# Kernel tuning notes

Hardware: AMD Instinct MI355X
Metric: run time of the kernel (lower is better)

The kernel has to match this reference:

```python
import jax, jax.numpy as jnp
import numpy as np

DIM = 1024
N_QUBITS = 10
NUM_LAYERS = 4
BATCH = 32768


def _build_cyclic_cnot(n_qubits):
    # Faithful replication of the torch build (which swaps each row pair
    # twice per control, so the result is the identity matrix).
    dim = 2 ** n_qubits
    cnot = np.eye(dim, dtype=np.float32)
    for control in range(n_qubits - 1):
        target = control + 1
        for i in range(dim):
            if (i >> control) & 1:
                j = i ^ (1 << target)
                cnot[[i, j], :] = cnot[[j, i], :]
    control, target = n_qubits - 1, 0
    for i in range(dim):
        if (i >> control) & 1:
            j = i ^ (1 << target)
            cnot[[i, j], :] = cnot[[j, i], :]
    return cnot


def setup_inputs() -> dict:
    key = jax.random.key(0)
    kx, ka = jax.random.split(key)
    x = jax.random.normal(kx, (BATCH, DIM), dtype=jnp.float32)
    local_angles = jax.random.normal(ka, (NUM_LAYERS, N_QUBITS, 3), dtype=jnp.float32)
    cnot_matrix = jnp.asarray(_build_cyclic_cnot(N_QUBITS))
    return {"x": x, "local_angles": local_angles, "cnot_matrix": cnot_matrix}


def _single_qubit_gates(angles):
    # angles: (L, n, 3) -> per-qubit 2x2 gate Rz @ Ry @ Rx, each R(t)=[[c,-s],[s,c]]
    h = angles * 0.5
    c, s = jnp.cos(h), jnp.sin(h)
    R = jnp.stack([jnp.stack([c, -s], axis=-1),
                   jnp.stack([s, c], axis=-1)], axis=-2)  # (L, n, 3, 2, 2)
    return jnp.einsum('lnij,lnjk,lnkm->lnim', R[:, :, 2], R[:, :, 1], R[:, :, 0])  # (L, n, 2, 2)


def _kron_all(mats):
    # mats: (n, 2, 2) -> dense (2^n, 2^n) Kronecker product, qubit 0 outermost
    out = mats[0]
    for q in range(1, mats.shape[0]):
        d = out.shape[0]
        out = jnp.einsum('ij,kl->ikjl', out, mats[q]).reshape(d * 2, d * 2)
    return out


def reference(x, local_angles, cnot_matrix):
    gates = _single_qubit_gates(local_angles)  # (L, n, 2, 2)
    out = x
    for l in range(local_angles.shape[0]):
        U = _kron_all(gates[l])  # (dim, dim)
        out = out @ U.T
        out = out @ cnot_matrix.T
    return out
```

## Files before the change

kernel.cpp:

```cpp
#include <hip/hip_runtime.h>
#include <math.h>

#define WPB 4
#define LDS_STRIDE 1184

__device__ __forceinline__ int padA(int i) {
    return i + ((i >> 5) << 2) + (((i >> 8) & 3) << 3) + (((i >> 6) & 3) << 2);
}

#define LGKM0() __asm__ volatile("s_waitcnt lgkmcnt(0)" ::: "memory")

__global__ __launch_bounds__(256) void qel_butterfly(
    const float* __restrict__ x,
    const float* __restrict__ ang,
    float* __restrict__ out,
    int rows)
{
    __shared__ __align__(16) float sm[WPB * LDS_STRIDE];
    const int tid  = threadIdx.x;
    const int wave = tid >> 6;
    const int lane = tid & 63;
    float* wsm = sm + wave * LDS_STRIDE;

    float cb[10], sb[10];
#pragma unroll
    for (int n = 0; n < 10; ++n) {
        float t = 0.f;
#pragma unroll
        for (int l = 0; l < 4; ++l) {
            const float* a = ang + (l * 10 + n) * 3;
            t += a[0] + a[1] + a[2];
        }
        t *= 0.5f;
        sincosf(t, &sb[9 - n], &cb[9 - n]);
    }

    const int waveId = blockIdx.x * WPB + wave;
    const int nW     = gridDim.x * WPB;

    for (int row = waveId; row < rows; row += nW) {
        const float* xr = x   + (size_t)row * 1024;
        float*       yr = out + (size_t)row * 1024;
        float v[16];

#define STAGE(P, CC, SS)                                        \
    do {                                                        \
        _Pragma("unroll")                                       \
        for (int q = 0; q < 16; ++q)                            \
            if ((q & (1 << (P))) == 0) {                        \
                float lo = v[q], hi = v[q | (1 << (P))];        \
                v[q]             = (CC) * lo - (SS) * hi;       \
                v[q | (1 << (P))] = (SS) * lo + (CC) * hi;      \
            }                                                   \
    } while (0)

#pragma unroll
        for (int m = 0; m < 4; ++m) {
            const float4 t4 = *(const float4*)(xr + 256 * m + 4 * lane);
            v[4*m+0] = t4.x; v[4*m+1] = t4.y; v[4*m+2] = t4.z; v[4*m+3] = t4.w;
        }
        STAGE(0, cb[0], sb[0]);
        STAGE(1, cb[1], sb[1]);
        STAGE(2, cb[8], sb[8]);
        STAGE(3, cb[9], sb[9]);

        LGKM0();
#pragma unroll
        for (int m = 0; m < 4; ++m) {
            float4 t4 = make_float4(v[4*m+0], v[4*m+1], v[4*m+2], v[4*m+3]);
            *(float4*)(wsm + padA(256 * m + 4 * lane)) = t4;
        }
        LGKM0();

        {
            const int g = lane >> 2, t = lane & 3;
#pragma unroll
            for (int j = 0; j < 16; ++j)
                v[j] = wsm[padA(64 * g + 4 * j + t)];
            STAGE(0, cb[2], sb[2]);
            STAGE(1, cb[3], sb[3]);
            STAGE(2, cb[4], sb[4]);
            STAGE(3, cb[5], sb[5]);
#pragma unroll
            for (int j = 0; j < 16; ++j)
                wsm[padA(64 * g + 4 * j + t)] = v[j];
        }
        LGKM0();

        {
            const int M = lane >> 4, L = lane & 15;
#pragma unroll
            for (int h = 0; h < 4; ++h) {
                const float4 t4 = *(const float4*)(wsm + padA(256 * M + 64 * h + 4 * L));
                v[4*h+0] = t4.x; v[4*h+1] = t4.y; v[4*h+2] = t4.z; v[4*h+3] = t4.w;
            }
            STAGE(2, cb[6], sb[6]);
            STAGE(3, cb[7], sb[7]);
#pragma unroll
            for (int h = 0; h < 4; ++h) {
                float4 t4 = make_float4(v[4*h+0], v[4*h+1], v[4*h+2], v[4*h+3]);
                *(float4*)(yr + 256 * M + 64 * h + 4 * L) = t4;
            }
        }
#undef STAGE
    }
}

extern "C" void kernel_launch(void* const* d_in, const int* in_sizes, int n_in,
                              void* d_out, int out_size, void* d_ws, size_t ws_size,
                              hipStream_t stream) {
    const float* x   = (const float*)d_in[0];
    const float* ang = (const float*)d_in[1];
    float* out = (float*)d_out;
    const int rows = in_sizes[0] / 1024;
    int blocks = (rows + WPB - 1) / WPB;
    if (blocks > 2048) blocks = 2048;
    qel_butterfly<<<blocks, 256, 0, stream>>>(x, ang, out, rows);
}
```

Measured before the change: 236.5 us.

## Use one row per wave, issue global loads before trig, nontemporal stores

Replaces the grid-stride loop (capped at 2048 blocks) with a launch of one row per wave across 8192 blocks. The four float4 global loads are now issued before the per-thread sincos setup so their latency overlaps the trig work. Output is written with nontemporal stores to reduce cache pollution. The explicit lgkmcnt waits between LDS phases are removed and left to the compiler, which should still order the same-wave LDS accesses correctly. The cost is redoing the angle sincos setup for every row instead of once per wave.

```diff
diff --git a/kernel.cpp b/kernel.cpp
--- a/kernel.cpp
+++ b/kernel.cpp
@@ -4,11 +4,11 @@
 #define WPB 4
 #define LDS_STRIDE 1184
 
+typedef float v4f __attribute__((ext_vector_type(4)));
+
 __device__ __forceinline__ int padA(int i) {
     return i + ((i >> 5) << 2) + (((i >> 8) & 3) << 3) + (((i >> 6) & 3) << 2);
 }
-
-#define LGKM0() __asm__ volatile("s_waitcnt lgkmcnt(0)" ::: "memory")
 
 __global__ __launch_bounds__(256) void qel_butterfly(
     const float* __restrict__ x,
@@ -21,6 +21,17 @@
     const int wave = tid >> 6;
     const int lane = tid & 63;
     float* wsm = sm + wave * LDS_STRIDE;
+
+    const int row = blockIdx.x * WPB + wave;
+    if (row >= rows) return;
+
+    const float* xr = x   + (size_t)row * 1024;
+    float*       yr = out + (size_t)row * 1024;
+
+    float4 L0 = *(const float4*)(xr +   0 + 4 * lane);
+    float4 L1 = *(const float4*)(xr + 256 + 4 * lane);
+    float4 L2 = *(const float4*)(xr + 512 + 4 * lane);
+    float4 L3 = *(const float4*)(xr + 768 + 4 * lane);
 
     float cb[10], sb[10];
 #pragma unroll
@@ -35,13 +46,7 @@
         sincosf(t, &sb[9 - n], &cb[9 - n]);
     }
 
-    const int waveId = blockIdx.x * WPB + wave;
-    const int nW     = gridDim.x * WPB;
-
-    for (int row = waveId; row < rows; row += nW) {
-        const float* xr = x   + (size_t)row * 1024;
-        float*       yr = out + (size_t)row * 1024;
-        float v[16];
+    float v[16];
 
 #define STAGE(P, CC, SS)                                        \
     do {                                                        \
@@ -49,61 +54,56 @@
         for (int q = 0; q < 16; ++q)                            \
             if ((q & (1 << (P))) == 0) {                        \
                 float lo = v[q], hi = v[q | (1 << (P))];        \
-                v[q]             = (CC) * lo - (SS) * hi;       \
+                v[q]              = (CC) * lo - (SS) * hi;      \
                 v[q | (1 << (P))] = (SS) * lo + (CC) * hi;      \
             }                                                   \
     } while (0)
 
+    v[0]=L0.x; v[1]=L0.y; v[2]=L0.z; v[3]=L0.w;
+    v[4]=L1.x; v[5]=L1.y; v[6]=L1.z; v[7]=L1.w;
+    v[8]=L2.x; v[9]=L2.y; v[10]=L2.z; v[11]=L2.w;
+    v[12]=L3.x; v[13]=L3.y; v[14]=L3.z; v[15]=L3.w;
+
+    STAGE(0, cb[0], sb[0]);
+    STAGE(1, cb[1], sb[1]);
+    STAGE(2, cb[8], sb[8]);
+    STAGE(3, cb[9], sb[9]);
+
 #pragma unroll
-        for (int m = 0; m < 4; ++m) {
-            const float4 t4 = *(const float4*)(xr + 256 * m + 4 * lane);
-            v[4*m+0] = t4.x; v[4*m+1] = t4.y; v[4*m+2] = t4.z; v[4*m+3] = t4.w;
+    for (int m = 0; m < 4; ++m)
+        *(float4*)(wsm + padA(256 * m + 4 * lane)) =
+            make_float4(v[4*m+0], v[4*m+1], v[4*m+2], v[4*m+3]);
+
+    {
+        const int g = lane >> 2, t = lane & 3;
+#pragma unroll
+        for (int j = 0; j < 16; ++j)
+            v[j] = wsm[padA(64 * g + 4 * j + t)];
+        STAGE(0, cb[2], sb[2]);
+        STAGE(1, cb[3], sb[3]);
+        STAGE(2, cb[4], sb[4]);
+        STAGE(3, cb[5], sb[5]);
+#pragma unroll
+        for (int j = 0; j < 16; ++j)
+            wsm[padA(64 * g + 4 * j + t)] = v[j];
+    }
+
+    {
+        const int M = lane >> 4, L = lane & 15;
+#pragma unroll
+        for (int h = 0; h < 4; ++h) {
+            const float4 t4 = *(const float4*)(wsm + padA(256 * M + 64 * h + 4 * L));
+            v[4*h+0] = t4.x; v[4*h+1] = t4.y; v[4*h+2] = t4.z; v[4*h+3] = t4.w;
         }
-        STAGE(0, cb[0], sb[0]);
-        STAGE(1, cb[1], sb[1]);
-        STAGE(2, cb[8], sb[8]);
-        STAGE(3, cb[9], sb[9]);
-
-        LGKM0();
+        STAGE(2, cb[6], sb[6]);
+        STAGE(3, cb[7], sb[7]);
 #pragma unroll
-        for (int m = 0; m < 4; ++m) {
-            float4 t4 = make_float4(v[4*m+0], v[4*m+1], v[4*m+2], v[4*m+3]);
-            *(float4*)(wsm + padA(256 * m + 4 * lane)) = t4;
+        for (int h = 0; h < 4; ++h) {
+            v4f t4 = { v[4*h+0], v[4*h+1], v[4*h+2], v[4*h+3] };
+            __builtin_nontemporal_store(t4, (v4f*)(yr + 256 * M + 64 * h + 4 * L));
         }
-        LGKM0();
-
-        {
-            const int g = lane >> 2, t = lane & 3;
-#pragma unroll
-            for (int j = 0; j < 16; ++j)
-                v[j] = wsm[padA(64 * g + 4 * j + t)];
-            STAGE(0, cb[2], sb[2]);
-            STAGE(1, cb[3], sb[3]);
-            STAGE(2, cb[4], sb[4]);
-            STAGE(3, cb[5], sb[5]);
-#pragma unroll
-            for (int j = 0; j < 16; ++j)
-                wsm[padA(64 * g + 4 * j + t)] = v[j];
-        }
-        LGKM0();
-
-        {
-            const int M = lane >> 4, L = lane & 15;
-#pragma unroll
-            for (int h = 0; h < 4; ++h) {
-                const float4 t4 = *(const float4*)(wsm + padA(256 * M + 64 * h + 4 * L));
-                v[4*h+0] = t4.x; v[4*h+1] = t4.y; v[4*h+2] = t4.z; v[4*h+3] = t4.w;
-            }
-            STAGE(2, cb[6], sb[6]);
-            STAGE(3, cb[7], sb[7]);
-#pragma unroll
-            for (int h = 0; h < 4; ++h) {
-                float4 t4 = make_float4(v[4*h+0], v[4*h+1], v[4*h+2], v[4*h+3]);
-                *(float4*)(yr + 256 * M + 64 * h + 4 * L) = t4;
-            }
-        }
+    }
 #undef STAGE
-    }
 }
 
 extern "C" void kernel_launch(void* const* d_in, const int* in_sizes, int n_in,
@@ -113,7 +113,6 @@
     const float* ang = (const float*)d_in[1];
     float* out = (float*)d_out;
     const int rows = in_sizes[0] / 1024;
-    int blocks = (rows + WPB - 1) / WPB;
-    if (blocks > 2048) blocks = 2048;
+    const int blocks = (rows + WPB - 1) / WPB;
     qel_butterfly<<<blocks, 256, 0, stream>>>(x, ang, out, rows);
 }
```

After: 236.8 us. No clear change (+0.1%).
